# Performance work log

Hardware: AMD Instinct MI355X
Metric: run time of the kernel (lower is better)

The kernel has to match this reference:

```python
import jax, jax.numpy as jnp
import numpy as np

N_EXPERTS, D_MODEL, D_FF, TOP_K, N_TOKENS = 8, 1024, 4096, 2, 8192

def _uniform_init(key, shape, fan_in):
    # matches torch init: gain = sqrt(1/3), std = gain/sqrt(fan_in), bound = sqrt(3)*std
    bound = np.sqrt(3.0) * np.sqrt(1.0 / 3.0) / np.sqrt(fan_in)
    return jax.random.uniform(key, shape, minval=-bound, maxval=bound, dtype=jnp.float32)

def setup_inputs() -> dict:
    key = jax.random.key(0)
    kx, ki, kw, k1, k2, k3 = jax.random.split(key, 6)
    x = jax.random.normal(kx, (N_TOKENS, D_MODEL), dtype=jnp.float32)
    expert_indices = jax.random.randint(ki, (N_TOKENS, TOP_K), 0, N_EXPERTS, dtype=jnp.int32)
    expert_weights = jax.random.uniform(kw, (N_TOKENS, TOP_K), dtype=jnp.float32)
    w1 = _uniform_init(k1, (N_EXPERTS, D_MODEL, D_FF), D_MODEL)
    w2 = _uniform_init(k2, (N_EXPERTS, D_MODEL, D_FF), D_MODEL)
    w3 = _uniform_init(k3, (N_EXPERTS, D_FF, D_MODEL), D_FF)
    return {"x": x, "expert_indices": expert_indices, "expert_weights": expert_weights,
            "w1": w1, "w2": w2, "w3": w3}

def reference(x, expert_indices, expert_weights, w1, w2, w3):
    # For each token t and routed expert e with routing weight p:
    #   out[t] += p * (silu(x[t] @ W1[e]) * (x[t] @ W2[e])) @ W3[e]
    # Loop over the small fixed expert set; compute each expert's SwiGLU FFN
    # densely over all tokens and combine with per-token routing weights
    # (mathematically identical to the sorted-dispatch grouped GEMM).
    n_experts = w1.shape[0]
    out = jnp.zeros_like(x)
    for e in range(n_experts):
        gate = x @ w1[e]                 # [N, d_ff]
        val = x @ w2[e]                  # [N, d_ff]
        y = (jax.nn.silu(gate) * val) @ w3[e]   # [N, d_model]
        # sum routing weights over top_k slots that picked expert e
        p = jnp.sum(jnp.where(expert_indices == e, expert_weights, 0.0), axis=1)
        out = out + p[:, None] * y
    return out
```

## Files before the change

### kernel.cpp

```cpp
#include <hip/hip_runtime.h>
#include <hip/hip_bf16.h>

typedef __attribute__((ext_vector_type(8))) short short8;
typedef __attribute__((ext_vector_type(4))) float f32x4;
typedef unsigned short u16;
typedef unsigned int u32;

#define NTOK   8192
#define DMODEL 1024
#define DFF    4096
#define NEXP   8
#define NPAIR  (NTOK * 2)
#define PADM   256
#define MT1    72
#define PPAD   (MT1 * PADM)
#define MT2    (PPAD / 128)

#define OFF_XB   0ull
#define OFF_W1T  (OFF_XB  + (size_t)NTOK * DMODEL * 2)
#define OFF_W2T  (OFF_W1T + (size_t)NEXP * DFF * DMODEL * 2)
#define OFF_W3T  (OFF_W2T + (size_t)NEXP * DFF * DMODEL * 2)
#define OFF_H    (OFF_W3T + (size_t)NEXP * DMODEL * DFF * 2)
#define OFF_TOK  (OFF_H   + (size_t)PPAD * DFF * 2)
#define OFF_WGT  (OFF_TOK + (size_t)PPAD * 4)
#define OFF_CNT  (OFF_WGT + (size_t)PPAD * 4)
#define OFF_CUR  (OFF_CNT + 64)
#define OFF_OFFP (OFF_CUR + 64)
#define WS_END   (OFF_OFFP + 64)

#define GLOAD16(gp, lp)                                                        \
  __builtin_amdgcn_global_load_lds(                                            \
      (const __attribute__((address_space(1))) u32*)(gp),                      \
      (__attribute__((address_space(3))) u32*)(lp), 16, 0, 0)

__device__ __forceinline__ u16 f2bu(float f) {
  __hip_bfloat16 b = __float2bfloat16(f);
  return __builtin_bit_cast(u16, b);
}


__global__ __launch_bounds__(256) void cvt_x_k(const float* __restrict__ x,
                                               u16* __restrict__ xb) {
  int i = blockIdx.x * 256 + threadIdx.x;
  float4 v = ((const float4*)x)[i];
  unsigned long long pk = (unsigned long long)f2bu(v.x) |
                          ((unsigned long long)f2bu(v.y) << 16) |
                          ((unsigned long long)f2bu(v.z) << 32) |
                          ((unsigned long long)f2bu(v.w) << 48);
  ((unsigned long long*)xb)[i] = pk;
}

__global__ __launch_bounds__(256) void tr_cvt_k(const float* __restrict__ src,
                                                u16* __restrict__ dst, int R, int C) {
  src += (size_t)blockIdx.z * R * C;
  dst += (size_t)blockIdx.z * R * C;
  int c0 = blockIdx.x * 64, r0 = blockIdx.y * 64;
  __shared__ float tile[64][65];
  int tid = threadIdx.x;
  int f4 = tid & 15, rr = tid >> 4;
#pragma unroll
  for (int p = 0; p < 4; ++p) {
    int r = rr + p * 16;
    float4 v = *(const float4*)(src + (size_t)(r0 + r) * C + c0 + f4 * 4);
    tile[r][f4 * 4 + 0] = v.x; tile[r][f4 * 4 + 1] = v.y;
    tile[r][f4 * 4 + 2] = v.z; tile[r][f4 * 4 + 3] = v.w;
  }
  __syncthreads();
  int ch = tid & 7, cc = tid >> 3;
#pragma unroll
  for (int p = 0; p < 2; ++p) {
    int c = cc + p * 32;
    short8 s;
#pragma unroll
    for (int j = 0; j < 8; ++j) s[j] = (short)f2bu(tile[ch * 8 + j][c]);
    *(short8*)(dst + (size_t)(c0 + c) * R + r0 + ch * 8) = s;
  }
}


__global__ __launch_bounds__(256) void count_k(const int* __restrict__ ei,
                                               int* __restrict__ cnt) {
  int i = blockIdx.x * 256 + threadIdx.x;
  atomicAdd(&cnt[ei[i]], 1);
}

__global__ void scan_k(const int* __restrict__ cnt, int* __restrict__ offp) {
  if (threadIdx.x == 0) {
    int a = 0;
#pragma unroll
    for (int e = 0; e < NEXP; ++e) { offp[e] = a; a += (cnt[e] + PADM - 1) & ~(PADM - 1); }
    offp[NEXP] = a;
  }
}

__global__ __launch_bounds__(256) void scatter_k(const int* __restrict__ ei,
                                                 const float* __restrict__ ew,
                                                 const int* __restrict__ offp,
                                                 int* __restrict__ cur,
                                                 int* __restrict__ tok,
                                                 float* __restrict__ wg) {
  int i = blockIdx.x * 256 + threadIdx.x;
  int e = ei[i];
  int p = offp[e] + atomicAdd(&cur[e], 1);
  tok[p] = i >> 1;
  wg[p] = ew[i];
}


#define A_STR 16384
#define B_STR 8192

__global__ __launch_bounds__(512, 2) void stage1_k(const u16* __restrict__ xb,
                                                   const u16* __restrict__ w1t,
                                                   const u16* __restrict__ w2t,
                                                   u16* __restrict__ h,
                                                   const int* __restrict__ tok,
                                                   const int* __restrict__ offp) {
  extern __shared__ __align__(16) u16 lds[];
  const int r0 = blockIdx.y * PADM;
  if (r0 >= offp[NEXP]) return;
  int e = 0;
#pragma unroll
  for (int q = 0; q < 7; ++q) e += (offp[e + 1] <= r0) ? 1 : 0;
  const int n0 = blockIdx.x * 128;
  const int tid = threadIdx.x;
  const int lane = tid & 63, w = tid >> 6;
  const int wm = w >> 2, wn = w & 3;
  const int lr = lane >> 3, seg = lane & 7;

  const u16* aga[4];
  int adb[4];
#pragma unroll
  for (int u = 0; u < 2; ++u)
#pragma unroll
    for (int j = 0; j < 2; ++j) {
      int row = u * 128 + w * 16 + j * 8 + lr;
      int t = tok[r0 + row];
      aga[u * 2 + j] = xb + (size_t)t * DMODEL + ((seg ^ (row & 7)) << 3);
      adb[u * 2 + j] = (u * 128 + w * 16 + j * 8) * 64;
    }
  const u16* w1e = w1t + (size_t)e * DFF * DMODEL;
  const u16* w2e = w2t + (size_t)e * DFF * DMODEL;
  const u16* bg1[2]; const u16* bg2[2];
  int bdb[2];
#pragma unroll
  for (int j = 0; j < 2; ++j) {
    int row = w * 16 + j * 8 + lr;
    size_t ro = (size_t)(n0 + row) * DMODEL + ((seg ^ (row & 7)) << 3);
    bg1[j] = w1e + ro; bg2[j] = w2e + ro;
    bdb[j] = (w * 16 + j * 8) * 64;
  }

  int aoff[8], boff[2];
  {
    int ks = lane >> 4;
#pragma unroll
    for (int mi = 0; mi < 8; ++mi) {
      int row = wm * 128 + mi * 16 + (lane & 15);
      aoff[mi] = row * 64 + ((ks ^ (row & 7)) << 3);
    }
#pragma unroll
    for (int ni = 0; ni < 2; ++ni) {
      int col = wn * 32 + ni * 16 + (lane & 15);
      boff[ni] = col * 64 + ((ks ^ (col & 7)) << 3);
    }
  }

  f32x4 accg[8][2], accv[8][2];
  const f32x4 zero = {0.f, 0.f, 0.f, 0.f};
#pragma unroll
  for (int mi = 0; mi < 8; ++mi)
#pragma unroll
    for (int ni = 0; ni < 2; ++ni) { accg[mi][ni] = zero; accv[mi][ni] = zero; }

  short8 af[4][2], bf1[2][2], bf2[2][2];

  {
    u16* Aq = lds; u16* B1q = lds + 2 * A_STR; u16* B2q = lds + 2 * A_STR + 2 * B_STR;
#pragma unroll
    for (int j = 0; j < 4; ++j) GLOAD16(aga[j], Aq + adb[j]);
#pragma unroll
    for (int j = 0; j < 2; ++j) { GLOAD16(bg1[j], B1q + bdb[j]);
                                  GLOAD16(bg2[j], B2q + bdb[j]); }
    asm volatile("s_waitcnt vmcnt(0)" ::: "memory");
    __builtin_amdgcn_s_barrier();
    __builtin_amdgcn_sched_barrier(0);
  }

#define S1_STEP(P, KC)                                                         \
  {                                                                            \
    const u16* Ab  = lds + (P) * A_STR;                                        \
    const u16* B1b = lds + 2 * A_STR + (P) * B_STR;                            \
    const u16* B2b = lds + 2 * A_STR + 2 * B_STR + (P) * B_STR;                \
    u16* Aq  = lds + (1 - (P)) * A_STR;                                        \
    u16* B1q = lds + 2 * A_STR + (1 - (P)) * B_STR;                            \
    u16* B2q = lds + 2 * A_STR + 2 * B_STR + (1 - (P)) * B_STR;                \
    const int st = (KC) + 1 < 16;                                              \
    const int ko = ((KC) + 1) * 64;                                            \
        \
    _Pragma("unroll") for (int mi = 0; mi < 4; ++mi)                           \
      _Pragma("unroll") for (int kk = 0; kk < 2; ++kk)                         \
        af[mi][kk] = *(const short8*)(Ab + (aoff[mi] ^ (kk << 5)));            \
    _Pragma("unroll") for (int ni = 0; ni < 2; ++ni)                           \
      _Pragma("unroll") for (int kk = 0; kk < 2; ++kk)                         \
        bf1[ni][kk] = *(const short8*)(B1b + (boff[ni] ^ (kk << 5)));          \
    if (st) {                                                                  \
      _Pragma("unroll") for (int j = 0; j < 4; ++j)                            \
        GLOAD16(aga[j] + ko, Aq + adb[j]);                                     \
      _Pragma("unroll") for (int j = 0; j < 2; ++j) {                          \
        GLOAD16(bg1[j] + ko, B1q + bdb[j]);                                    \
        GLOAD16(bg2[j] + ko, B2q + bdb[j]);                                    \
      }                                                                        \
    }                                                                          \
    __builtin_amdgcn_s_barrier();                                              \
    __builtin_amdgcn_s_setprio(1);                                             \
    _Pragma("unroll") for (int mi = 0; mi < 4; ++mi)                           \
      _Pragma("unroll") for (int ni = 0; ni < 2; ++ni)                         \
        _Pragma("unroll") for (int kk = 0; kk < 2; ++kk)                       \
          accg[mi][ni] = __builtin_amdgcn_mfma_f32_16x16x32_bf16(              \
              af[mi][kk], bf1[ni][kk], accg[mi][ni], 0, 0, 0);                 \
    __builtin_amdgcn_s_setprio(0);                                             \
    __builtin_amdgcn_s_barrier();                                              \
                                       \
    _Pragma("unroll") for (int ni = 0; ni < 2; ++ni)                           \
      _Pragma("unroll") for (int kk = 0; kk < 2; ++kk)                         \
        bf2[ni][kk] = *(const short8*)(B2b + (boff[ni] ^ (kk << 5)));          \
    __builtin_amdgcn_s_barrier();                                              \
    __builtin_amdgcn_s_setprio(1);                                             \
    _Pragma("unroll") for (int mi = 0; mi < 4; ++mi)                           \
      _Pragma("unroll") for (int ni = 0; ni < 2; ++ni)                         \
        _Pragma("unroll") for (int kk = 0; kk < 2; ++kk)                       \
          accv[mi][ni] = __builtin_amdgcn_mfma_f32_16x16x32_bf16(              \
              af[mi][kk], bf2[ni][kk], accv[mi][ni], 0, 0, 0);                 \
    __builtin_amdgcn_s_setprio(0);                                             \
    __builtin_amdgcn_s_barrier();                                              \
      \
    _Pragma("unroll") for (int mi = 0; mi < 4; ++mi)                           \
      _Pragma("unroll") for (int kk = 0; kk < 2; ++kk)                         \
        af[mi][kk] = *(const short8*)(Ab + (aoff[4 + mi] ^ (kk << 5)));        \
    __builtin_amdgcn_s_barrier();                                              \
    __builtin_amdgcn_s_setprio(1);                                             \
    _Pragma("unroll") for (int mi = 0; mi < 4; ++mi)                           \
      _Pragma("unroll") for (int ni = 0; ni < 2; ++ni)                         \
        _Pragma("unroll") for (int kk = 0; kk < 2; ++kk)                       \
          accg[4 + mi][ni] = __builtin_amdgcn_mfma_f32_16x16x32_bf16(          \
              af[mi][kk], bf1[ni][kk], accg[4 + mi][ni], 0, 0, 0);             \
    _Pragma("unroll") for (int mi = 0; mi < 4; ++mi)                           \
      _Pragma("unroll") for (int ni = 0; ni < 2; ++ni)                         \
        _Pragma("unroll") for (int kk = 0; kk < 2; ++kk)                       \
          accv[4 + mi][ni] = __builtin_amdgcn_mfma_f32_16x16x32_bf16(          \
              af[mi][kk], bf2[ni][kk], accv[4 + mi][ni], 0, 0, 0);             \
    __builtin_amdgcn_s_setprio(0);                                             \
    asm volatile("s_waitcnt vmcnt(0)" ::: "memory");                           \
    __builtin_amdgcn_s_barrier();                                              \
    __builtin_amdgcn_sched_barrier(0);                                         \
  }

  for (int kc = 0; kc < 16; kc += 2) {
    S1_STEP(0, kc)
    S1_STEP(1, kc + 1)
  }
#undef S1_STEP

  const int prow = r0 + wm * 128 + ((lane >> 4) << 2);
  const int pcol = n0 + wn * 32 + (lane & 15);
#pragma unroll
  for (int mi = 0; mi < 8; ++mi)
#pragma unroll
    for (int ni = 0; ni < 2; ++ni)
#pragma unroll
      for (int j = 0; j < 4; ++j) {
        float g = accg[mi][ni][j];
        float v = accv[mi][ni][j];
        float s = g / (1.f + __expf(-g));
        h[(size_t)(prow + mi * 16 + j) * DFF + (pcol + ni * 16)] = f2bu(s * v);
      }
}


__global__ __launch_bounds__(256) void stage2_k(const u16* __restrict__ h,
                                                const u16* __restrict__ w3t,
                                                float* __restrict__ out,
                                                const int* __restrict__ tok,
                                                const float* __restrict__ wg,
                                                const int* __restrict__ offp) {
  __shared__ __align__(16) u16 As[128 * 64];
  __shared__ __align__(16) u16 Bs[64 * 64];
  const int r0 = blockIdx.y * 128;
  if (r0 >= offp[NEXP]) return;
  int e = 0;
#pragma unroll
  for (int q = 0; q < 7; ++q) e += (offp[e + 1] <= r0) ? 1 : 0;
  const int n0 = blockIdx.x * 64;
  const int tid = threadIdx.x;
  const int lane = tid & 63, w = tid >> 6;
  const int wm = w >> 1, wn = w & 1;
  const int lr = lane >> 3, seg = lane & 7;

  const u16* aga[4];
#pragma unroll
  for (int j = 0; j < 4; ++j) {
    int rowl = w * 32 + j * 8 + lr;
    aga[j] = h + (size_t)(r0 + rowl) * DFF + ((seg ^ (rowl & 7)) << 3);
  }
  const u16* w3e = w3t + (size_t)e * DMODEL * DFF;
  const u16* bga[2];
#pragma unroll
  for (int j = 0; j < 2; ++j) {
    int coll = w * 16 + j * 8 + lr;
    bga[j] = w3e + (size_t)(n0 + coll) * DFF + ((seg ^ (coll & 7)) << 3);
  }
  u16 *Ad[4], *Bd[2];
#pragma unroll
  for (int j = 0; j < 4; ++j) Ad[j] = As + (w * 32 + j * 8) * 64;
#pragma unroll
  for (int j = 0; j < 2; ++j) Bd[j] = Bs + (w * 16 + j * 8) * 64;

  int aoff[4][2], boff[2][2];
  {
    int ar = wm * 64 + (lane & 15), ks = lane >> 4;
#pragma unroll
    for (int mi = 0; mi < 4; ++mi)
#pragma unroll
      for (int kk = 0; kk < 2; ++kk) {
        int row = ar + mi * 16;
        aoff[mi][kk] = row * 64 + (((kk * 4 + ks) ^ (row & 7)) << 3);
      }
    int bc = wn * 32 + (lane & 15);
#pragma unroll
    for (int ni = 0; ni < 2; ++ni)
#pragma unroll
      for (int kk = 0; kk < 2; ++kk) {
        int col = bc + ni * 16;
        boff[ni][kk] = col * 64 + (((kk * 4 + ks) ^ (col & 7)) << 3);
      }
  }

  f32x4 acc[4][2];
  const f32x4 zero = {0.f, 0.f, 0.f, 0.f};
#pragma unroll
  for (int mi = 0; mi < 4; ++mi)
#pragma unroll
    for (int ni = 0; ni < 2; ++ni) acc[mi][ni] = zero;

  for (int kc = 0; kc < DFF / 64; ++kc) {
    const int ko = kc * 64;
#pragma unroll
    for (int j = 0; j < 4; ++j) GLOAD16(aga[j] + ko, Ad[j]);
#pragma unroll
    for (int j = 0; j < 2; ++j) GLOAD16(bga[j] + ko, Bd[j]);
    __syncthreads();
#pragma unroll
    for (int kk = 0; kk < 2; ++kk) {
      short8 a[4], b[2];
#pragma unroll
      for (int mi = 0; mi < 4; ++mi) a[mi] = *(const short8*)(As + aoff[mi][kk]);
#pragma unroll
      for (int ni = 0; ni < 2; ++ni) b[ni] = *(const short8*)(Bs + boff[ni][kk]);
#pragma unroll
      for (int mi = 0; mi < 4; ++mi)
#pragma unroll
        for (int ni = 0; ni < 2; ++ni)
          acc[mi][ni] = __builtin_amdgcn_mfma_f32_16x16x32_bf16(a[mi], b[ni], acc[mi][ni], 0, 0, 0);
    }
    __syncthreads();
  }

  const int prow = r0 + wm * 64 + ((lane >> 4) << 2);
  const int pcol = n0 + wn * 32 + (lane & 15);
#pragma unroll
  for (int mi = 0; mi < 4; ++mi)
#pragma unroll
    for (int j = 0; j < 4; ++j) {
      int pos = prow + mi * 16 + j;
      float p = wg[pos];
      if (p != 0.f) {
        int t = tok[pos];
#pragma unroll
        for (int ni = 0; ni < 2; ++ni)
          atomicAdd(&out[(size_t)t * DMODEL + pcol + ni * 16], p * acc[mi][ni][j]);
      }
    }
}


extern "C" void kernel_launch(void* const* d_in, const int* in_sizes, int n_in,
                              void* d_out, int out_size, void* d_ws, size_t ws_size,
                              hipStream_t stream) {
  (void)in_sizes; (void)n_in;
  const float* x  = (const float*)d_in[0];
  const int*   ei = (const int*)d_in[1];
  const float* ew = (const float*)d_in[2];
  const float* w1 = (const float*)d_in[3];
  const float* w2 = (const float*)d_in[4];
  const float* w3 = (const float*)d_in[5];
  float* out = (float*)d_out;
  char* ws = (char*)d_ws;

  hipMemsetAsync(out, 0, (size_t)out_size * sizeof(float), stream);
  if (ws_size < WS_END) return;

  u16* xb   = (u16*)(ws + OFF_XB);
  u16* w1t  = (u16*)(ws + OFF_W1T);
  u16* w2t  = (u16*)(ws + OFF_W2T);
  u16* w3t  = (u16*)(ws + OFF_W3T);
  u16* hb   = (u16*)(ws + OFF_H);
  int* tok  = (int*)(ws + OFF_TOK);
  float* wg = (float*)(ws + OFF_WGT);
  int* cnt  = (int*)(ws + OFF_CNT);
  int* cur  = (int*)(ws + OFF_CUR);
  int* offp = (int*)(ws + OFF_OFFP);

  hipMemsetAsync(ws + OFF_TOK, 0, (size_t)(WS_END - OFF_TOK), stream);

  hipFuncSetAttribute(reinterpret_cast<const void*>(stage1_k),
                      hipFuncAttributeMaxDynamicSharedMemorySize, 131072);

  cvt_x_k<<<dim3(NTOK * DMODEL / 4 / 256), 256, 0, stream>>>(x, xb);
  tr_cvt_k<<<dim3(DFF / 64, DMODEL / 64, NEXP), 256, 0, stream>>>(w1, w1t, DMODEL, DFF);
  tr_cvt_k<<<dim3(DFF / 64, DMODEL / 64, NEXP), 256, 0, stream>>>(w2, w2t, DMODEL, DFF);
  tr_cvt_k<<<dim3(DMODEL / 64, DFF / 64, NEXP), 256, 0, stream>>>(w3, w3t, DFF, DMODEL);
  count_k<<<dim3(NPAIR / 256), 256, 0, stream>>>(ei, cnt);
  scan_k<<<1, 64, 0, stream>>>(cnt, offp);
  scatter_k<<<dim3(NPAIR / 256), 256, 0, stream>>>(ei, ew, offp, cur, tok, wg);
  stage1_k<<<dim3(DFF / 128, MT1), 512, 131072, stream>>>(xb, w1t, w2t, hb, tok, offp);
  stage2_k<<<dim3(DMODEL / 64, MT2), 256, 0, stream>>>(hb, w3t, out, tok, wg, offp);
}
```

Before: 860.2 us.

## Triple-buffer stage1 GEMM with K=32 tiles and fewer barriers

Restructures the stage1 gate/value GEMM main loop. The old loop used a K=64 tile, double buffering and several barriers per step. The new loop uses a K=32 tile with a three-buffer LDS ring, keeps two global loads in flight (vmcnt(4)), and has one barrier per step. LDS per block drops from 128KB to 96KB, and the A fragments are loaded all at once with 8 registers. Each step now does half as much MFMA work, so per-iteration overhead relative to compute goes up, and the deeper prefetch may not fully hide load latency.

Result: faster. 842.5 us (-2.1%).

```diff
diff --git a/kernel.cpp b/kernel.cpp
--- a/kernel.cpp
+++ b/kernel.cpp
@@ -107,8 +107,8 @@
 }
 
 
-#define A_STR 16384
-#define B_STR 8192
+#define S1_BUF 16384
+#define S1_NK  32
 
 __global__ __launch_bounds__(512, 2) void stage1_k(const u16* __restrict__ xb,
                                                    const u16* __restrict__ w1t,
@@ -126,29 +126,26 @@
   const int tid = threadIdx.x;
   const int lane = tid & 63, w = tid >> 6;
   const int wm = w >> 2, wn = w & 3;
-  const int lr = lane >> 3, seg = lane & 7;
-
-  const u16* aga[4];
-  int adb[4];
-#pragma unroll
-  for (int u = 0; u < 2; ++u)
-#pragma unroll
-    for (int j = 0; j < 2; ++j) {
-      int row = u * 128 + w * 16 + j * 8 + lr;
-      int t = tok[r0 + row];
-      aga[u * 2 + j] = xb + (size_t)t * DMODEL + ((seg ^ (row & 7)) << 3);
-      adb[u * 2 + j] = (u * 128 + w * 16 + j * 8) * 64;
-    }
+
+  const int sl = lane & 3, rl = lane >> 2;
+  const u16* aga[2];
+  int adb[2];
+#pragma unroll
+  for (int j = 0; j < 2; ++j) {
+    int row = w * 32 + j * 16 + rl;
+    int t = tok[r0 + row];
+    aga[j] = xb + (size_t)t * DMODEL + ((sl ^ ((row >> 1) & 3)) << 3);
+    adb[j] = (w * 32 + j * 16) * 32;
+  }
   const u16* w1e = w1t + (size_t)e * DFF * DMODEL;
   const u16* w2e = w2t + (size_t)e * DFF * DMODEL;
-  const u16* bg1[2]; const u16* bg2[2];
-  int bdb[2];
-#pragma unroll
-  for (int j = 0; j < 2; ++j) {
-    int row = w * 16 + j * 8 + lr;
-    size_t ro = (size_t)(n0 + row) * DMODEL + ((seg ^ (row & 7)) << 3);
-    bg1[j] = w1e + ro; bg2[j] = w2e + ro;
-    bdb[j] = (w * 16 + j * 8) * 64;
+  const u16* bg1; const u16* bg2;
+  int bdb;
+  {
+    int row = w * 16 + rl;
+    size_t ro = (size_t)(n0 + row) * DMODEL + ((sl ^ ((row >> 1) & 3)) << 3);
+    bg1 = w1e + ro; bg2 = w2e + ro;
+    bdb = (w * 16) * 32;
   }
 
   int aoff[8], boff[2];
@@ -157,12 +154,12 @@
 #pragma unroll
     for (int mi = 0; mi < 8; ++mi) {
       int row = wm * 128 + mi * 16 + (lane & 15);
-      aoff[mi] = row * 64 + ((ks ^ (row & 7)) << 3);
+      aoff[mi] = row * 32 + ((ks ^ ((row >> 1) & 3)) << 3);
     }
 #pragma unroll
     for (int ni = 0; ni < 2; ++ni) {
       int col = wn * 32 + ni * 16 + (lane & 15);
-      boff[ni] = col * 64 + ((ks ^ (col & 7)) << 3);
+      boff[ni] = col * 32 + ((ks ^ ((col >> 1) & 3)) << 3);
     }
   }
 
@@ -173,94 +170,57 @@
 #pragma unroll
     for (int ni = 0; ni < 2; ++ni) { accg[mi][ni] = zero; accv[mi][ni] = zero; }
 
-  short8 af[4][2], bf1[2][2], bf2[2][2];
-
-  {
-    u16* Aq = lds; u16* B1q = lds + 2 * A_STR; u16* B2q = lds + 2 * A_STR + 2 * B_STR;
-#pragma unroll
-    for (int j = 0; j < 4; ++j) GLOAD16(aga[j], Aq + adb[j]);
-#pragma unroll
-    for (int j = 0; j < 2; ++j) { GLOAD16(bg1[j], B1q + bdb[j]);
-                                  GLOAD16(bg2[j], B2q + bdb[j]); }
-    asm volatile("s_waitcnt vmcnt(0)" ::: "memory");
-    __builtin_amdgcn_s_barrier();
-    __builtin_amdgcn_sched_barrier(0);
-  }
-
-#define S1_STEP(P, KC)                                                         \
+#define S1_ISSUE(Q, KO)                                                        \
+  do {                                                                         \
+    GLOAD16(aga[0] + (KO), (Q) + adb[0]);                                      \
+    GLOAD16(aga[1] + (KO), (Q) + adb[1]);                                      \
+    GLOAD16(bg1 + (KO), (Q) + 8192 + bdb);                                     \
+    GLOAD16(bg2 + (KO), (Q) + 12288 + bdb);                                    \
+  } while (0)
+
+  S1_ISSUE(lds, 0);
+  S1_ISSUE(lds + S1_BUF, 32);
+  asm volatile("s_waitcnt vmcnt(4)" ::: "memory");
+  __builtin_amdgcn_s_barrier();
+  __builtin_amdgcn_sched_barrier(0);
+
+#define S1_STEP(P, KC, ISSUE)                                                  \
   {                                                                            \
-    const u16* Ab  = lds + (P) * A_STR;                                        \
-    const u16* B1b = lds + 2 * A_STR + (P) * B_STR;                            \
-    const u16* B2b = lds + 2 * A_STR + 2 * B_STR + (P) * B_STR;                \
-    u16* Aq  = lds + (1 - (P)) * A_STR;                                        \
-    u16* B1q = lds + 2 * A_STR + (1 - (P)) * B_STR;                            \
-    u16* B2q = lds + 2 * A_STR + 2 * B_STR + (1 - (P)) * B_STR;                \
-    const int st = (KC) + 1 < 16;                                              \
-    const int ko = ((KC) + 1) * 64;                                            \
-        \
-    _Pragma("unroll") for (int mi = 0; mi < 4; ++mi)                           \
-      _Pragma("unroll") for (int kk = 0; kk < 2; ++kk)                         \
-        af[mi][kk] = *(const short8*)(Ab + (aoff[mi] ^ (kk << 5)));            \
-    _Pragma("unroll") for (int ni = 0; ni < 2; ++ni)                           \
-      _Pragma("unroll") for (int kk = 0; kk < 2; ++kk)                         \
-        bf1[ni][kk] = *(const short8*)(B1b + (boff[ni] ^ (kk << 5)));          \
-    if (st) {                                                                  \
-      _Pragma("unroll") for (int j = 0; j < 4; ++j)                            \
-        GLOAD16(aga[j] + ko, Aq + adb[j]);                                     \
-      _Pragma("unroll") for (int j = 0; j < 2; ++j) {                          \
-        GLOAD16(bg1[j] + ko, B1q + bdb[j]);                                    \
-        GLOAD16(bg2[j] + ko, B2q + bdb[j]);                                    \
+    const u16* Ab  = lds + (P) * S1_BUF;                                       \
+    const u16* B1b = Ab + 8192;                                                \
+    const u16* B2b = Ab + 12288;                                               \
+    short8 af[8], b1f[2], b2f[2];                                              \
+    _Pragma("unroll") for (int mi = 0; mi < 8; ++mi)                           \
+      af[mi] = *(const short8*)(Ab + aoff[mi]);                                \
+    _Pragma("unroll") for (int ni = 0; ni < 2; ++ni) {                         \
+      b1f[ni] = *(const short8*)(B1b + boff[ni]);                              \
+      b2f[ni] = *(const short8*)(B2b + boff[ni]);                              \
+    }                                                                          \
+    if (ISSUE) S1_ISSUE(lds + (((P) + 2) % 3) * S1_BUF, ((KC) + 2) * 32);      \
+    __builtin_amdgcn_s_setprio(1);                                             \
+    _Pragma("unroll") for (int mi = 0; mi < 8; ++mi)                           \
+      _Pragma("unroll") for (int ni = 0; ni < 2; ++ni) {                       \
+        accg[mi][ni] = __builtin_amdgcn_mfma_f32_16x16x32_bf16(                \
+            af[mi], b1f[ni], accg[mi][ni], 0, 0, 0);                           \
+        accv[mi][ni] = __builtin_amdgcn_mfma_f32_16x16x32_bf16(                \
+            af[mi], b2f[ni], accv[mi][ni], 0, 0, 0);                           \
       }                                                                        \
-    }                                                                          \
-    __builtin_amdgcn_s_barrier();                                              \
-    __builtin_amdgcn_s_setprio(1);                                             \
-    _Pragma("unroll") for (int mi = 0; mi < 4; ++mi)                           \
-      _Pragma("unroll") for (int ni = 0; ni < 2; ++ni)                         \
-        _Pragma("unroll") for (int kk = 0; kk < 2; ++kk)                       \
-          accg[mi][ni] = __builtin_amdgcn_mfma_f32_16x16x32_bf16(              \
-              af[mi][kk], bf1[ni][kk], accg[mi][ni], 0, 0, 0);                 \
     __builtin_amdgcn_s_setprio(0);                                             \
-    __builtin_amdgcn_s_barrier();                                              \
-                                       \
-    _Pragma("unroll") for (int ni = 0; ni < 2; ++ni)                           \
-      _Pragma("unroll") for (int kk = 0; kk < 2; ++kk)                         \
-        bf2[ni][kk] = *(const short8*)(B2b + (boff[ni] ^ (kk << 5)));          \
-    __builtin_amdgcn_s_barrier();                                              \
-    __builtin_amdgcn_s_setprio(1);                                             \
-    _Pragma("unroll") for (int mi = 0; mi < 4; ++mi)                           \
-      _Pragma("unroll") for (int ni = 0; ni < 2; ++ni)                         \
-        _Pragma("unroll") for (int kk = 0; kk < 2; ++kk)                       \
-          accv[mi][ni] = __builtin_amdgcn_mfma_f32_16x16x32_bf16(              \
-              af[mi][kk], bf2[ni][kk], accv[mi][ni], 0, 0, 0);                 \
-    __builtin_amdgcn_s_setprio(0);                                             \
-    __builtin_amdgcn_s_barrier();                                              \
-      \
-    _Pragma("unroll") for (int mi = 0; mi < 4; ++mi)                           \
-      _Pragma("unroll") for (int kk = 0; kk < 2; ++kk)                         \
-        af[mi][kk] = *(const short8*)(Ab + (aoff[4 + mi] ^ (kk << 5)));        \
-    __builtin_amdgcn_s_barrier();                                              \
-    __builtin_amdgcn_s_setprio(1);                                             \
-    _Pragma("unroll") for (int mi = 0; mi < 4; ++mi)                           \
-      _Pragma("unroll") for (int ni = 0; ni < 2; ++ni)                         \
-        _Pragma("unroll") for (int kk = 0; kk < 2; ++kk)                       \
-          accg[4 + mi][ni] = __builtin_amdgcn_mfma_f32_16x16x32_bf16(          \
-              af[mi][kk], bf1[ni][kk], accg[4 + mi][ni], 0, 0, 0);             \
-    _Pragma("unroll") for (int mi = 0; mi < 4; ++mi)                           \
-      _Pragma("unroll") for (int ni = 0; ni < 2; ++ni)                         \
-        _Pragma("unroll") for (int kk = 0; kk < 2; ++kk)                       \
-          accv[4 + mi][ni] = __builtin_amdgcn_mfma_f32_16x16x32_bf16(          \
-              af[mi][kk], bf2[ni][kk], accv[4 + mi][ni], 0, 0, 0);             \
-    __builtin_amdgcn_s_setprio(0);                                             \
-    asm volatile("s_waitcnt vmcnt(0)" ::: "memory");                           \
+    if (ISSUE) asm volatile("s_waitcnt vmcnt(4)" ::: "memory");                \
+    else       asm volatile("s_waitcnt vmcnt(0)" ::: "memory");                \
     __builtin_amdgcn_s_barrier();                                              \
     __builtin_amdgcn_sched_barrier(0);                                         \
   }
 
-  for (int kc = 0; kc < 16; kc += 2) {
-    S1_STEP(0, kc)
-    S1_STEP(1, kc + 1)
-  }
+  for (int kc = 0; kc < S1_NK - 2; kc += 3) {
+    S1_STEP(0, kc, 1)
+    S1_STEP(1, kc + 1, 1)
+    S1_STEP(2, kc + 2, 1)
+  }
+  S1_STEP(0, S1_NK - 2, 0)
+  S1_STEP(1, S1_NK - 1, 0)
 #undef S1_STEP
+#undef S1_ISSUE
 
   const int prow = r0 + wm * 128 + ((lane >> 4) << 2);
   const int pcol = n0 + wn * 32 + (lane & 15);
@@ -414,7 +374,7 @@
   hipMemsetAsync(ws + OFF_TOK, 0, (size_t)(WS_END - OFF_TOK), stream);
 
   hipFuncSetAttribute(reinterpret_cast<const void*>(stage1_k),
-                      hipFuncAttributeMaxDynamicSharedMemorySize, 131072);
+                      hipFuncAttributeMaxDynamicSharedMemorySize, 98304);
 
   cvt_x_k<<<dim3(NTOK * DMODEL / 4 / 256), 256, 0, stream>>>(x, xb);
   tr_cvt_k<<<dim3(DFF / 64, DMODEL / 64, NEXP), 256, 0, stream>>>(w1, w1t, DMODEL, DFF);
@@ -423,6 +383,6 @@
   count_k<<<dim3(NPAIR / 256), 256, 0, stream>>>(ei, cnt);
   scan_k<<<1, 64, 0, stream>>>(cnt, offp);
   scatter_k<<<dim3(NPAIR / 256), 256, 0, stream>>>(ei, ew, offp, cur, tok, wg);
-  stage1_k<<<dim3(DFF / 128, MT1), 512, 131072, stream>>>(xb, w1t, w2t, hb, tok, offp);
+  stage1_k<<<dim3(DFF / 128, MT1), 512, 98304, stream>>>(xb, w1t, w2t, hb, tok, offp);
   stage2_k<<<dim3(DMODEL / 64, MT2), 256, 0, stream>>>(hb, w3t, out, tok, wg, offp);
 }
```
